# Performance work log

Hardware: AMD Instinct MI355X
Metric: run time of the kernel (lower is better)

Reference implementation:

```python
import jax, jax.numpy as jnp
import numpy as np


def _grid_sample_bilinear(img, grid):
    # img: [B,C,H,W]; grid: [B,Hg,Wg,2] normalized to [-1,1] (x,y), align_corners=False,
    # zero padding (torch F.grid_sample defaults).
    B, C, H, W = img.shape
    Hg, Wg = grid.shape[1], grid.shape[2]
    gx, gy = grid[..., 0], grid[..., 1]
    ix = (gx + 1.0) * (W * 0.5) - 0.5
    iy = (gy + 1.0) * (H * 0.5) - 0.5
    ix0 = jnp.floor(ix)
    iy0 = jnp.floor(iy)
    tx = (ix - ix0).reshape(B, 1, -1)
    ty = (iy - iy0).reshape(B, 1, -1)
    img_flat = img.reshape(B, C, H * W)

    def corner(xi, yi):
        valid = ((xi >= 0) & (xi < W) & (yi >= 0) & (yi < H)).reshape(B, 1, -1)
        xc = jnp.clip(xi, 0, W - 1).astype(jnp.int32)
        yc = jnp.clip(yi, 0, H - 1).astype(jnp.int32)
        idx = (yc * W + xc).reshape(B, -1)                      # [B, Hg*Wg]
        vals = jax.vmap(lambda f, i: f[:, i])(img_flat, idx)    # [B, C, Hg*Wg]
        return vals * valid

    v00 = corner(ix0, iy0)
    v01 = corner(ix0 + 1, iy0)
    v10 = corner(ix0, iy0 + 1)
    v11 = corner(ix0 + 1, iy0 + 1)
    out = (v00 * (1 - tx) * (1 - ty) + v01 * tx * (1 - ty)
           + v10 * (1 - tx) * ty + v11 * tx * ty)
    return out.reshape(B, C, Hg, Wg)


def setup_inputs() -> dict:
    key = jax.random.key(0)
    ks = jax.random.split(key, 8)
    B, C, RHO, WP = 32, 384, 25, 256
    HC, WC = 64, 64
    D = 2 * C  # 768, channels after polar/cart concat
    std = 0.02
    return {
        "polar_feat": jax.random.normal(ks[0], (B, C, RHO, WP), jnp.float32),
        "cart_feat": jax.random.normal(ks[1], (B, C, HC, WC), jnp.float32),
        "grid": jax.random.uniform(ks[2], (B, RHO, WP, 2), jnp.float32, -1.0, 1.0),
        "W1_0": jax.random.normal(ks[3], (D, 40), jnp.float32) * std,
        "b1_0": jnp.zeros((40,), jnp.float32),
        "W2_0": jax.random.normal(ks[4], (40, 1), jnp.float32) * std,
        "b2_0": jnp.zeros((1,), jnp.float32),
        "W1s": jax.random.normal(ks[5], (24, D + 1, 40), jnp.float32) * std,
        "b1s": jnp.zeros((24, 40), jnp.float32),
        "W2s": jax.random.normal(ks[6], (24, 40, 1), jnp.float32) * std,
        "b2s": jnp.zeros((24, 1), jnp.float32),
    }


def reference(polar_feat, cart_feat, grid, W1_0, b1_0, W2_0, b2_0, W1s, b1s, W2s, b2s):
    # Polar grid-sample fusion of cartesian features onto the polar grid.
    fe_cart_p = _grid_sample_bilinear(cart_feat, grid)              # [B,C,25,Wp]
    fe_cat_p = jnp.concatenate([polar_feat, fe_cart_p], axis=1)     # [B,768,25,Wp]
    # AdaptiveAvgPool2d((None,1)): mean over width.
    fe = jnp.mean(fe_cat_p, axis=3)                                 # [B,768,25]

    feats = jnp.transpose(fe, (2, 0, 1))                            # [25,B,768]
    gelu = lambda x: jax.nn.gelu(x, approximate=False)

    # Head 0: no recurrent input.
    h0 = gelu(feats[0] @ W1_0 + b1_0)
    out0 = h0 @ W2_0 + b2_0                                         # [B,1]

    # Heads 1..24: concat previous scalar output before first linear (fully_local=False).
    def step(out_prev, xs):
        feat, W1, b1, W2, b2 = xs
        x = jnp.concatenate([feat, out_prev], axis=-1)              # [B,769]
        h = gelu(x @ W1 + b1)
        o = h @ W2 + b2                                             # [B,1]
        return o, o

    _, outs = jax.lax.scan(step, out0, (feats[1:], W1s, b1s, W2s, b2s))
    out = jnp.concatenate([out0[None], outs], axis=0)               # [25,B,1]
    out = jnp.transpose(out[:, :, 0], (1, 0))                       # [B,25]
    return jnp.clip(out, 0.0, jnp.pi)
```

## Files before the change

kernel.cpp:

```cpp
#include <hip/hip_runtime.h>
#include <math.h>

#define B_    32
#define C_    384
#define RHO_  25
#define WP_   256
#define PIX_  4096
#define D_    768
#define HID_  40
#define NROWS (B_*C_*RHO_)
#define FE_N (RHO_*B_*D_)
#define POLARBLK 2048

__device__ __forceinline__ float gelu_exact(float x) {
    return 0.5f * x * (1.f + erff(x * 0.70710678118654752f));
}

__global__ __launch_bounds__(256) void front_kernel(const float* __restrict__ polar,
        const float* __restrict__ grid,
        const float* __restrict__ W1_0, const float* __restrict__ W1s,
        float* __restrict__ bins, float* __restrict__ W1T, float* __restrict__ fe) {
    __shared__ float lb[PIX_];
    int tid = threadIdx.x;
    int bid = blockIdx.x;
    if (bid < POLARBLK) {
        int wid = bid * 4 + (tid >> 6);
        int lane = tid & 63;
        const int NW = POLARBLK * 4;
        for (int r0 = wid; r0 < NROWS; r0 += 4 * NW) {
            float s[4];
            #pragma unroll
            for (int k = 0; k < 4; ++k) {
                int r = r0 + k * NW;
                float4 v = (r < NROWS) ? ((const float4*)(polar + (size_t)r * WP_))[lane]
                                       : make_float4(0.f, 0.f, 0.f, 0.f);
                s[k] = v.x + v.y + v.z + v.w;
            }
            #pragma unroll
            for (int m = 32; m >= 1; m >>= 1) {
                #pragma unroll
                for (int k = 0; k < 4; ++k) s[k] += __shfl_xor(s[k], m, 64);
            }
            if (lane == 0) {
                #pragma unroll
                for (int k = 0; k < 4; ++k) {
                    int r = r0 + k * NW;
                    if (r < NROWS) {
                        int rho = r % RHO_, cch = (r / RHO_) % C_, bb = r / (RHO_ * C_);
                        fe[((size_t)(rho * B_ + bb)) * D_ + cch] = s[k] * (1.f / 256.f);
                    }
                }
            }
        }
    } else if (bid < POLARBLK + B_ * RHO_) {
        int bb = bid - POLARBLK;
        for (int i = tid; i < PIX_ / 4; i += 256) ((float4*)lb)[i] = make_float4(0.f, 0.f, 0.f, 0.f);
        __syncthreads();
        int pt = bb * WP_ + tid;
        float2 g = ((const float2*)grid)[pt];
        float ix = (g.x + 1.f) * 32.f - 0.5f;
        float iy = (g.y + 1.f) * 32.f - 0.5f;
        float x0f = floorf(ix), y0f = floorf(iy);
        float fx = ix - x0f, fy = iy - y0f;
        int x0 = (int)x0f, y0 = (int)y0f;
        const float s = 1.f / 256.f;
        if ((unsigned)x0 < 64u) {
            if ((unsigned)y0 < 64u)       atomicAdd(&lb[y0 * 64 + x0],       (1.f - fx) * (1.f - fy) * s);
            if ((unsigned)(y0 + 1) < 64u) atomicAdd(&lb[(y0 + 1) * 64 + x0], (1.f - fx) * fy * s);
        }
        if ((unsigned)(x0 + 1) < 64u) {
            if ((unsigned)y0 < 64u)       atomicAdd(&lb[y0 * 64 + x0 + 1],       fx * (1.f - fy) * s);
            if ((unsigned)(y0 + 1) < 64u) atomicAdd(&lb[(y0 + 1) * 64 + x0 + 1], fx * fy * s);
        }
        __syncthreads();
        float4* dst = (float4*)(bins + (size_t)bb * PIX_);
        for (int i = tid; i < PIX_ / 4; i += 256) dst[i] = ((float4*)lb)[i];
    } else if (bid < POLARBLK + B_ * RHO_ + 25) {
        int i = bid - (POLARBLK + B_ * RHO_);
        const float* src = (i == 0) ? W1_0 : (W1s + (size_t)(i - 1) * 769 * HID_);
        float* dst = W1T + (size_t)i * HID_ * D_;
        for (int idx = tid; idx < HID_ * D_; idx += 256) {
            int j = idx / D_, c = idx % D_;
            dst[idx] = src[c * HID_ + j];
        }
    } else {
        int z = bid - (POLARBLK + B_ * RHO_ + 25);
        for (int i = tid; i < 16 * 96; i += 256) {
            int row = z * 16 + (i / 96), e = i % 96;
            ((float4*)fe)[(size_t)row * 192 + 96 + e] = make_float4(0.f, 0.f, 0.f, 0.f);
        }
    }
}

__global__ __launch_bounds__(256) void cart_kernel(const float* __restrict__ cart,
        const float* __restrict__ bins, float* __restrict__ fe) {
    __shared__ float ldsW[6400];
    int tid = threadIdx.x;
    int bid = blockIdx.x;
    int b   = bid / 48;
    int rem = bid % 48;
    int ct  = rem >> 3;
    int pg  = rem & 7;

    const float* binb = bins + (size_t)b * RHO_ * PIX_ + pg * 512;
    {
        const float4* b4 = (const float4*)binb;
        #pragma unroll 2
        for (int i = tid; i < 1600; i += 256) {
            int r = i >> 6, e = i & 63;
            ((float4*)ldsW)[(r << 6) + e] = b4[(size_t)r * 1024 + e];
        }
    }
    __syncthreads();

    int w = tid >> 6, lane = tid & 63;
    int j = lane >> 3, q = lane & 7;
    int c0 = ct * 64 + w * 8 + j;
    const float* xp0 = cart + ((size_t)b * C_ + c0) * PIX_ + pg * 512 + q * 4;
    const float* xp1 = xp0 + (size_t)32 * PIX_;

    float acc0[25], acc1[25];
    #pragma unroll
    for (int r = 0; r < 25; ++r) { acc0[r] = 0.f; acc1[r] = 0.f; }

    float4 a0 = *(const float4*)(xp0);
    float4 a1 = *(const float4*)(xp0 + 32);
    float4 b0 = *(const float4*)(xp1);
    float4 b1 = *(const float4*)(xp1 + 32);
    for (int t = 0; t < 16; ++t) {
        if (t == 8) {
            __syncthreads();
            const float4* b4 = (const float4*)(binb + 256);
            #pragma unroll 2
            for (int i = tid; i < 1600; i += 256) {
                int r = i >> 6, e = i & 63;
                ((float4*)ldsW)[(r << 6) + e] = b4[(size_t)r * 1024 + e];
            }
            __syncthreads();
        }
        float4 xa = a0, xb = b0;
        a0 = a1; b0 = b1;
        if (t < 14) {
            a1 = *(const float4*)(xp0 + (t + 2) * 32);
            b1 = *(const float4*)(xp1 + (t + 2) * 32);
        }
        const float* wb = ldsW + (t & 7) * 32 + q * 4;
        #pragma unroll
        for (int r = 0; r < 25; ++r) {
            float4 wv = *(const float4*)(wb + (r << 8));
            acc0[r] += xa.x * wv.x + xa.y * wv.y + xa.z * wv.z + xa.w * wv.w;
            acc1[r] += xb.x * wv.x + xb.y * wv.y + xb.z * wv.z + xb.w * wv.w;
        }
    }
    #pragma unroll
    for (int r = 0; r < 25; ++r) {
        acc0[r] += __shfl_xor(acc0[r], 1, 64);
        acc0[r] += __shfl_xor(acc0[r], 2, 64);
        acc0[r] += __shfl_xor(acc0[r], 4, 64);
        acc1[r] += __shfl_xor(acc1[r], 1, 64);
        acc1[r] += __shfl_xor(acc1[r], 2, 64);
        acc1[r] += __shfl_xor(acc1[r], 4, 64);
    }
    __syncthreads();
    if (q == 0) {
        #pragma unroll
        for (int r = 0; r < 25; ++r) {
            ldsW[r * 64 + w * 8 + j]      = acc0[r];
            ldsW[r * 64 + 32 + w * 8 + j] = acc1[r];
        }
    }
    __syncthreads();
    for (int oi = tid; oi < 1600; oi += 256) {
        int r = oi >> 6, cc = oi & 63;
        atomicAdd(&fe[((size_t)(r * B_ + b)) * D_ + 384 + ct * 64 + cc], ldsW[oi]);
    }
}

__global__ __launch_bounds__(256) void mlp_pre_kernel(const float* __restrict__ fe,
        const float* __restrict__ W1T, const float* __restrict__ b1_0,
        const float* __restrict__ b1s, float* __restrict__ G) {
    int lane = threadIdx.x & 63;
    int trip = blockIdx.x * 4 + (threadIdx.x >> 6);
    int jh = trip & 1;
    int pair = trip >> 1;
    int i = pair >> 5, b = pair & 31;
    const float4* f4p = (const float4*)(fe + (size_t)(i * B_ + b) * D_);
    float4 f0 = f4p[lane], f1 = f4p[lane + 64], f2 = f4p[lane + 128];
    int j0 = jh * 20;
    #pragma unroll 2
    for (int j = j0; j < j0 + 20; ++j) {
        const float4* w4p = (const float4*)(W1T + ((size_t)i * HID_ + j) * D_);
        float4 w0 = w4p[lane], w1 = w4p[lane + 64], w2 = w4p[lane + 128];
        float s = f0.x*w0.x + f0.y*w0.y + f0.z*w0.z + f0.w*w0.w
                + f1.x*w1.x + f1.y*w1.y + f1.z*w1.z + f1.w*w1.w
                + f2.x*w2.x + f2.y*w2.y + f2.z*w2.z + f2.w*w2.w;
        #pragma unroll
        for (int m = 32; m >= 1; m >>= 1) s += __shfl_xor(s, m, 64);
        if (lane == 0) {
            float bias = (i == 0) ? b1_0[j] : b1s[(i - 1) * HID_ + j];
            G[(size_t)(i * B_ + b) * HID_ + j] = s + bias;
        }
    }
}

__global__ __launch_bounds__(64) void mlp_seq_kernel(const float* __restrict__ G,
        const float* __restrict__ W1s, const float* __restrict__ W2_0,
        const float* __restrict__ b2_0, const float* __restrict__ W2s,
        const float* __restrict__ b2s, float* __restrict__ out) {
    int lane = threadIdx.x;
    int j2 = lane & 31, b = blockIdx.x * 2 + (lane >> 5);
    bool hi = (j2 < 8);
    float g1[25], g2[25], wl1[25], wl2[25], w2a[25], w2b[25], bsc[25];
    #pragma unroll
    for (int i = 0; i < 25; ++i) {
        g1[i] = G[(size_t)(i * B_ + b) * HID_ + j2];
        g2[i] = hi ? G[(size_t)(i * B_ + b) * HID_ + 32 + j2] : 0.f;
    }
    wl1[0] = 0.f; wl2[0] = 0.f;
    w2a[0] = W2_0[j2]; w2b[0] = hi ? W2_0[32 + j2] : 0.f; bsc[0] = b2_0[0];
    #pragma unroll
    for (int i = 1; i < 25; ++i) {
        size_t base = ((size_t)(i - 1) * 769 + 768) * HID_;
        wl1[i] = W1s[base + j2];
        wl2[i] = hi ? W1s[base + 32 + j2] : 0.f;
        w2a[i] = W2s[(i - 1) * HID_ + j2];
        w2b[i] = hi ? W2s[(i - 1) * HID_ + 32 + j2] : 0.f;
        bsc[i] = b2s[i - 1];
    }
    float op = 0.f;
    #pragma unroll
    for (int i = 0; i < 25; ++i) {
        float x1 = g1[i] + op * wl1[i];
        float x2 = g2[i] + op * wl2[i];
        float p = gelu_exact(x1) * w2a[i] + gelu_exact(x2) * w2b[i];
        #pragma unroll
        for (int m = 16; m >= 1; m >>= 1) p += __shfl_xor(p, m, 64);
        float o = p + bsc[i];
        op = o;
        if (j2 == 0) out[b * 25 + i] = fminf(fmaxf(o, 0.f), 3.14159265358979323846f);
    }
}

extern "C" void kernel_launch(void* const* d_in, const int* in_sizes, int n_in,
                              void* d_out, int out_size, void* d_ws, size_t ws_size,
                              hipStream_t stream) {
    const float* polar = (const float*)d_in[0];
    const float* cart  = (const float*)d_in[1];
    const float* grid  = (const float*)d_in[2];
    const float* W1_0  = (const float*)d_in[3];
    const float* b1_0  = (const float*)d_in[4];
    const float* W2_0  = (const float*)d_in[5];
    const float* b2_0  = (const float*)d_in[6];
    const float* W1s   = (const float*)d_in[7];
    const float* b1s   = (const float*)d_in[8];
    const float* W2s   = (const float*)d_in[9];
    const float* b2s   = (const float*)d_in[10];
    float* out = (float*)d_out;

    float* bins = (float*)d_ws;
    float* fe   = bins + (size_t)B_ * RHO_ * PIX_;
    float* G    = fe + (size_t)FE_N;
    float* W1T  = G + (size_t)RHO_ * B_ * HID_;

    front_kernel<<<POLARBLK + B_ * RHO_ + 25 + 50, 256, 0, stream>>>(polar, grid, W1_0, W1s, bins, W1T, fe);
    cart_kernel<<<1536, 256, 0, stream>>>(cart, bins, fe);
    mlp_pre_kernel<<<(RHO_ * B_ * 2) / 4, 256, 0, stream>>>(fe, W1T, b1_0, b1s, G);
    mlp_seq_kernel<<<B_ / 2, 64, 0, stream>>>(G, W1s, W2_0, b2_0, W2s, b2s, out);
}
```

Measured before the change: 179.0 us.

## Compute cartesian bin projection with split-fp16 MFMA instead of FP32 FMA

```diff
diff --git a/kernel.cpp b/kernel.cpp
--- a/kernel.cpp
+++ b/kernel.cpp
@@ -11,6 +11,11 @@
 #define NROWS (B_*C_*RHO_)
 #define FE_N (RHO_*B_*D_)
 #define POLARBLK 2048
+#define PCH 8
+
+typedef _Float16 half_t;
+typedef __attribute__((ext_vector_type(8))) _Float16 half8;
+typedef __attribute__((ext_vector_type(4))) float f32x4;
 
 __device__ __forceinline__ float gelu_exact(float x) {
     return 0.5f * x * (1.f + erff(x * 0.70710678118654752f));
@@ -19,7 +24,8 @@
 __global__ __launch_bounds__(256) void front_kernel(const float* __restrict__ polar,
         const float* __restrict__ grid,
         const float* __restrict__ W1_0, const float* __restrict__ W1s,
-        float* __restrict__ bins, float* __restrict__ W1T, float* __restrict__ fe) {
+        half_t* __restrict__ Whi, half_t* __restrict__ Wlo,
+        float* __restrict__ W1T, float* __restrict__ fe) {
     __shared__ float lb[PIX_];
     int tid = threadIdx.x;
     int bid = blockIdx.x;
@@ -73,8 +79,15 @@
             if ((unsigned)(y0 + 1) < 64u) atomicAdd(&lb[(y0 + 1) * 64 + x0 + 1], fx * fy * s);
         }
         __syncthreads();
-        float4* dst = (float4*)(bins + (size_t)bb * PIX_);
-        for (int i = tid; i < PIX_ / 4; i += 256) dst[i] = ((float4*)lb)[i];
+        int b = bb / RHO_, rho = bb % RHO_;
+        half_t* wh = Whi + ((size_t)(b * 32 + rho)) * PIX_;
+        half_t* wl = Wlo + ((size_t)(b * 32 + rho)) * PIX_;
+        for (int i = tid; i < PIX_; i += 256) {
+            float wv = lb[i];
+            half_t h = (half_t)wv;
+            wh[i] = h;
+            wl[i] = (half_t)(wv - (float)h);
+        }
     } else if (bid < POLARBLK + B_ * RHO_ + 25) {
         int i = bid - (POLARBLK + B_ * RHO_);
         const float* src = (i == 0) ? W1_0 : (W1s + (size_t)(i - 1) * 769 * HID_);
@@ -92,87 +105,75 @@
     }
 }
 
-__global__ __launch_bounds__(256) void cart_kernel(const float* __restrict__ cart,
-        const float* __restrict__ bins, float* __restrict__ fe) {
-    __shared__ float ldsW[6400];
+__global__ __launch_bounds__(256) void cart_mfma_kernel(const float* __restrict__ cart,
+        const half_t* __restrict__ Whi, const half_t* __restrict__ Wlo,
+        float* __restrict__ fe) {
+    __shared__ float lds_out[1600];
     int tid = threadIdx.x;
     int bid = blockIdx.x;
-    int b   = bid / 48;
-    int rem = bid % 48;
-    int ct  = rem >> 3;
-    int pg  = rem & 7;
-
-    const float* binb = bins + (size_t)b * RHO_ * PIX_ + pg * 512;
-    {
-        const float4* b4 = (const float4*)binb;
-        #pragma unroll 2
-        for (int i = tid; i < 1600; i += 256) {
-            int r = i >> 6, e = i & 63;
-            ((float4*)ldsW)[(r << 6) + e] = b4[(size_t)r * 1024 + e];
-        }
-    }
-    __syncthreads();
-
+    int b  = bid / (6 * PCH);
+    int ct = (bid / PCH) % 6;
+    int pc = bid % PCH;
     int w = tid >> 6, lane = tid & 63;
-    int j = lane >> 3, q = lane & 7;
-    int c0 = ct * 64 + w * 8 + j;
-    const float* xp0 = cart + ((size_t)b * C_ + c0) * PIX_ + pg * 512 + q * 4;
-    const float* xp1 = xp0 + (size_t)32 * PIX_;
-
-    float acc0[25], acc1[25];
-    #pragma unroll
-    for (int r = 0; r < 25; ++r) { acc0[r] = 0.f; acc1[r] = 0.f; }
-
-    float4 a0 = *(const float4*)(xp0);
-    float4 a1 = *(const float4*)(xp0 + 32);
-    float4 b0 = *(const float4*)(xp1);
-    float4 b1 = *(const float4*)(xp1 + 32);
+    int row16 = lane & 15, kg = lane >> 4;
+
+    const float*  xrow = cart + ((size_t)b * C_ + ct * 64 + w * 16 + row16) * PIX_ + pc * 512 + kg * 8;
+    const half_t* bh0 = Whi + ((size_t)(b * 32 + row16)) * PIX_ + pc * 512 + kg * 8;
+    const half_t* bh1 = Whi + ((size_t)(b * 32 + 16 + row16)) * PIX_ + pc * 512 + kg * 8;
+    const half_t* bl0 = Wlo + ((size_t)(b * 32 + row16)) * PIX_ + pc * 512 + kg * 8;
+    const half_t* bl1 = Wlo + ((size_t)(b * 32 + 16 + row16)) * PIX_ + pc * 512 + kg * 8;
+
+    f32x4 acc0 = {0.f, 0.f, 0.f, 0.f};
+    f32x4 acc1 = {0.f, 0.f, 0.f, 0.f};
+
+    float4 xa = *(const float4*)(xrow);
+    float4 xb = *(const float4*)(xrow + 4);
+    half8 nbh0 = *(const half8*)(bh0);
+    half8 nbh1 = *(const half8*)(bh1);
+    half8 nbl0 = *(const half8*)(bl0);
+    half8 nbl1 = *(const half8*)(bl1);
+
     for (int t = 0; t < 16; ++t) {
-        if (t == 8) {
-            __syncthreads();
-            const float4* b4 = (const float4*)(binb + 256);
-            #pragma unroll 2
-            for (int i = tid; i < 1600; i += 256) {
-                int r = i >> 6, e = i & 63;
-                ((float4*)ldsW)[(r << 6) + e] = b4[(size_t)r * 1024 + e];
-            }
-            __syncthreads();
-        }
-        float4 xa = a0, xb = b0;
-        a0 = a1; b0 = b1;
-        if (t < 14) {
-            a1 = *(const float4*)(xp0 + (t + 2) * 32);
-            b1 = *(const float4*)(xp1 + (t + 2) * 32);
-        }
-        const float* wb = ldsW + (t & 7) * 32 + q * 4;
-        #pragma unroll
-        for (int r = 0; r < 25; ++r) {
-            float4 wv = *(const float4*)(wb + (r << 8));
-            acc0[r] += xa.x * wv.x + xa.y * wv.y + xa.z * wv.z + xa.w * wv.w;
-            acc1[r] += xb.x * wv.x + xb.y * wv.y + xb.z * wv.z + xb.w * wv.w;
-        }
-    }
-    #pragma unroll
-    for (int r = 0; r < 25; ++r) {
-        acc0[r] += __shfl_xor(acc0[r], 1, 64);
-        acc0[r] += __shfl_xor(acc0[r], 2, 64);
-        acc0[r] += __shfl_xor(acc0[r], 4, 64);
-        acc1[r] += __shfl_xor(acc1[r], 1, 64);
-        acc1[r] += __shfl_xor(acc1[r], 2, 64);
-        acc1[r] += __shfl_xor(acc1[r], 4, 64);
-    }
-    __syncthreads();
-    if (q == 0) {
-        #pragma unroll
-        for (int r = 0; r < 25; ++r) {
-            ldsW[r * 64 + w * 8 + j]      = acc0[r];
-            ldsW[r * 64 + 32 + w * 8 + j] = acc1[r];
-        }
+        float4 cxa = xa, cxb = xb;
+        half8 vbh0 = nbh0, vbh1 = nbh1, vbl0 = nbl0, vbl1 = nbl1;
+        if (t < 15) {
+            int off = (t + 1) * 32;
+            xa = *(const float4*)(xrow + off);
+            xb = *(const float4*)(xrow + off + 4);
+            nbh0 = *(const half8*)(bh0 + off);
+            nbh1 = *(const half8*)(bh1 + off);
+            nbl0 = *(const half8*)(bl0 + off);
+            nbl1 = *(const half8*)(bl1 + off);
+        }
+        float xs[8] = {cxa.x, cxa.y, cxa.z, cxa.w, cxb.x, cxb.y, cxb.z, cxb.w};
+        half8 ah, al;
+        #pragma unroll
+        for (int i = 0; i < 8; ++i) {
+            half_t h = (half_t)xs[i];
+            ah[i] = h;
+            al[i] = (half_t)(xs[i] - (float)h);
+        }
+        acc0 = __builtin_amdgcn_mfma_f32_16x16x32_f16(ah, vbh0, acc0, 0, 0, 0);
+        acc0 = __builtin_amdgcn_mfma_f32_16x16x32_f16(ah, vbl0, acc0, 0, 0, 0);
+        acc0 = __builtin_amdgcn_mfma_f32_16x16x32_f16(al, vbh0, acc0, 0, 0, 0);
+        acc1 = __builtin_amdgcn_mfma_f32_16x16x32_f16(ah, vbh1, acc1, 0, 0, 0);
+        acc1 = __builtin_amdgcn_mfma_f32_16x16x32_f16(ah, vbl1, acc1, 0, 0, 0);
+        acc1 = __builtin_amdgcn_mfma_f32_16x16x32_f16(al, vbh1, acc1, 0, 0, 0);
+    }
+
+    #pragma unroll
+    for (int r = 0; r < 4; ++r)
+        lds_out[(lane & 15) * 64 + w * 16 + kg * 4 + r] = acc0[r];
+    int rho1 = 16 + (lane & 15);
+    if (rho1 < RHO_) {
+        #pragma unroll
+        for (int r = 0; r < 4; ++r)
+            lds_out[rho1 * 64 + w * 16 + kg * 4 + r] = acc1[r];
     }
     __syncthreads();
     for (int oi = tid; oi < 1600; oi += 256) {
         int r = oi >> 6, cc = oi & 63;
-        atomicAdd(&fe[((size_t)(r * B_ + b)) * D_ + 384 + ct * 64 + cc], ldsW[oi]);
+        atomicAdd(&fe[((size_t)(r * B_ + b)) * D_ + 384 + ct * 64 + cc], lds_out[oi]);
     }
 }
 
@@ -257,13 +258,14 @@
     const float* b2s   = (const float*)d_in[10];
     float* out = (float*)d_out;
 
-    float* bins = (float*)d_ws;
-    float* fe   = bins + (size_t)B_ * RHO_ * PIX_;
+    half_t* Whi = (half_t*)d_ws;
+    half_t* Wlo = Whi + (size_t)B_ * 32 * PIX_;
+    float* fe   = (float*)(Wlo + (size_t)B_ * 32 * PIX_);
     float* G    = fe + (size_t)FE_N;
     float* W1T  = G + (size_t)RHO_ * B_ * HID_;
 
-    front_kernel<<<POLARBLK + B_ * RHO_ + 25 + 50, 256, 0, stream>>>(polar, grid, W1_0, W1s, bins, W1T, fe);
-    cart_kernel<<<1536, 256, 0, stream>>>(cart, bins, fe);
+    front_kernel<<<POLARBLK + B_ * RHO_ + 25 + 50, 256, 0, stream>>>(polar, grid, W1_0, W1s, Whi, Wlo, W1T, fe);
+    cart_mfma_kernel<<<B_ * 6 * PCH, 256, 0, stream>>>(cart, Whi, Wlo, fe);
     mlp_pre_kernel<<<(RHO_ * B_ * 2) / 4, 256, 0, stream>>>(fe, W1T, b1_0, b1s, G);
     mlp_seq_kernel<<<B_ / 2, 64, 0, stream>>>(G, W1s, W2_0, b2_0, W2s, b2s, out);
 }
```

Result: slower. 198.3 us (+10.8%).
